# Optimization experiments

Hardware: AMD Instinct MI355X
Metric: run time of the kernel (lower is better)

## Reference

```python
import jax, jax.numpy as jnp
import numpy as np

K = 8        # number of nearest neighbors
STRIDE = 1
PAD = 2      # 'same' padding for kernel_size=5


def setup_inputs() -> dict:
    key = jax.random.key(0)
    k1, k2, k3 = jax.random.split(key, 3)
    x = jax.random.normal(k1, (32, 3, 64, 64), dtype=jnp.float32)
    patches = jax.random.normal(k2, (2048, 3, 5, 5), dtype=jnp.float32)
    values = jax.random.normal(k3, (2048, 128), dtype=jnp.float32)
    return {"x": x, "patches": patches, "values": values}


def reference(x, patches, values):
    # Precompute (as done in NeighborsValuesAssigner.__init__):
    #   kernel = -patches, bias = 0.5 * ||patch||^2
    n = patches.shape[0]
    pf = patches.reshape(n, -1)
    bias = 0.5 * jnp.sum(pf * pf, axis=1)          # (N,)
    kernel = -patches                               # (N, C, kh, kw)

    # distances[b, n, h, w] = -<patch_n, x_patch(b,h,w)> + 0.5*||patch_n||^2
    dist = jax.lax.conv_general_dilated(
        x, kernel,
        window_strides=(STRIDE, STRIDE),
        padding=[(PAD, PAD), (PAD, PAD)],
        dimension_numbers=("NCHW", "OIHW", "NCHW"),
    ) + bias[None, :, None, None]                   # (B, N, H, W)

    # k smallest distances along the dictionary axis
    dist = jnp.transpose(dist, (0, 2, 3, 1))        # (B, H, W, N)
    _, idx = jax.lax.top_k(-dist, K)                # (B, H, W, K)

    # gather neighbor value vectors and mean-reduce over neighbors
    gathered = values[idx]                          # (B, H, W, K, D)
    out = jnp.mean(gathered, axis=3)                # (B, H, W, D)
    return jnp.transpose(out, (0, 3, 1, 2))         # (B, D, H, W)
```

## Files before the change

kernel.cpp:

```cpp
#include <hip/hip_runtime.h>
#include <float.h>

#define B_  32
#define C_  3
#define H_  64
#define W_  64
#define N_  2048
#define D_  128
#define KNN 8
#define PS  75
#define TILES 128
#define CK  12

typedef __attribute__((ext_vector_type(8))) _Float16 kh8;
typedef __attribute__((ext_vector_type(4))) float kvf4;

__global__ __launch_bounds__(256) void bias_kernel(const float* __restrict__ patches,
                                                   float* __restrict__ nbias) {
  int n = blockIdx.x * 256 + threadIdx.x;
  if (n < N_) {
    const float* __restrict__ p = patches + n * PS;
    float s = 0.f;
#pragma unroll
    for (int j = 0; j < PS; j++) s += p[j] * p[j];
    nbias[n] = -0.5f * s;
  }
}

__device__ __forceinline__ void bub12(unsigned (&s)[CK], unsigned c) {
#pragma unroll
  for (int j = 0; j < CK; j++) {
    const unsigned lo = s[j] < c ? s[j] : c;
    const unsigned hi = s[j] < c ? c : s[j];
    s[j] = lo;
    c = hi;
  }
}

__device__ __forceinline__ void ins8(float cd, int ci, float (&rd)[KNN], int (&ri)[KNN]) {
#pragma unroll
  for (int q = 0; q < KNN; q++) {
    const bool sw = (cd < rd[q]) || (cd == rd[q] && ci < ri[q]);
    const float nd = sw ? rd[q] : cd;
    const int   ni = sw ? ri[q] : ci;
    rd[q] = sw ? cd : rd[q];
    ri[q] = sw ? ci : ri[q];
    cd = nd;
    ci = ni;
  }
}

__global__ __launch_bounds__(256)
__attribute__((amdgpu_waves_per_eu(2, 4)))
void knn_kernel(const float* __restrict__ x, const float* __restrict__ patches,
                const float* __restrict__ values, const float* __restrict__ nbias,
                float* __restrict__ out) {
  __shared__ float xt[1633];
  __shared__ float mg_d[4][4][16][KNN];
  __shared__ int   mg_i[4][4][16][KNN];
  __shared__ int   bc_i[4][16][KNN];

  const int tid = threadIdx.x;
  const int bp = blockIdx.x * 256;
  const int b  = bp >> 12;
  const int h0 = (bp >> 6) & 63;

  for (int f = tid; f < 1632; f += 256) {
    const int c   = f / 544;
    const int rem = f - c * 544;
    const int j   = rem / 68;
    const int col = rem - j * 68;
    const int gr = h0 - 2 + j;
    const int gc = col - 2;
    float v = 0.f;
    if ((unsigned)gr < 64u && (unsigned)gc < 64u)
      v = x[((b * 3 + c) * 64 + gr) * 64 + gc];
    xt[f] = v;
  }
  if (tid == 0) xt[1632] = 0.f;
  __syncthreads();

  const int lane = tid & 63;
  const int wid  = tid >> 6;
  const int l15  = lane & 15;
  const int g4   = lane >> 4;

  kh8 bfr[4][3];
  float snorm[4];
#pragma unroll
  for (int g = 0; g < 4; g++) {
    const int pb = wid * 68 + g * 16 + l15;
#pragma unroll
    for (int s = 0; s < 3; s++) {
      union { _Float16 h[8]; kh8 v; } fr;
#pragma unroll
      for (int i = 0; i < 8; i++) {
        const int k  = s * 32 + g4 * 8 + i;
        const int c  = k / 25;
        const int r2 = k - c * 25;
        const int addr = (k < PS) ? (pb + c * 544 + (r2 / 5) * 68 + (r2 % 5)) : 1632;
        fr.h[i] = (_Float16)xt[addr];
      }
      bfr[g][s] = fr.v;
    }
    float sq = 0.f;
#pragma unroll
    for (int c = 0; c < 3; c++)
#pragma unroll
      for (int dh = 0; dh < 5; dh++)
#pragma unroll
        for (int dw = 0; dw < 5; dw++) {
          const _Float16 hv = (_Float16)xt[pb + c * 544 + dh * 68 + dw];
          const float vr = (float)hv;
          sq = fmaf(vr, vr, sq);
        }
    snorm[g] = 0.5f * sq;
  }

  unsigned sk0[CK], sk1[CK], sk2[CK], sk3[CK];
#pragma unroll
  for (int j = 0; j < CK; j++) sk0[j] = sk1[j] = sk2[j] = sk3[j] = 0xFFFFFFFFu;

#pragma unroll 1
  for (int t = 0; t < TILES; t++) {
    const float* __restrict__ pr = patches + (t * 16 + l15) * PS + g4 * 8;
    union { _Float16 h[8]; kh8 v; } af[3];
#pragma unroll
    for (int s = 0; s < 3; s++)
#pragma unroll
      for (int i = 0; i < 8; i++) {
        const int k = s * 32 + g4 * 8 + i;
        const float e = (k < PS) ? pr[s * 32 + i] : 0.f;
        af[s].h[i] = (_Float16)e;
      }

    const int nbb = t * 16 + g4 * 4;
    const float nb0 = nbias[nbb + 0];
    const float nb1 = nbias[nbb + 1];
    const float nb2 = nbias[nbb + 2];
    const float nb3 = nbias[nbb + 3];
    const unsigned tb = (unsigned)nbb;
#pragma unroll
    for (int g = 0; g < 4; g++) {
      kvf4 acc;
      acc[0] = nb0; acc[1] = nb1; acc[2] = nb2; acc[3] = nb3;
      acc = __builtin_amdgcn_mfma_f32_16x16x32_f16(af[0].v, bfr[g][0], acc, 0, 0, 0);
      acc = __builtin_amdgcn_mfma_f32_16x16x32_f16(af[1].v, bfr[g][1], acc, 0, 0, 0);
      acc = __builtin_amdgcn_mfma_f32_16x16x32_f16(af[2].v, bfr[g][2], acc, 0, 0, 0);
#pragma unroll
      for (int r = 0; r < 4; r++) {
        float kv = snorm[g] - acc[r];
        kv = fmaxf(kv, 0.f);
        const unsigned ku = (__float_as_uint(kv) & 0xFFFFF800u) | (tb + (unsigned)r);
        if      (g == 0) bub12(sk0, ku);
        else if (g == 1) bub12(sk1, ku);
        else if (g == 2) bub12(sk2, ku);
        else             bub12(sk3, ku);
      }
    }
  }

#pragma unroll 1
  for (int g = 0; g < 4; g++) {
    float xv[PS];
    const int pb = wid * 68 + g * 16 + l15;
#pragma unroll
    for (int c = 0; c < 3; c++)
#pragma unroll
      for (int dh = 0; dh < 5; dh++)
#pragma unroll
        for (int dw = 0; dw < 5; dw++)
          xv[(c * 5 + dh) * 5 + dw] = xt[pb + c * 544 + dh * 68 + dw];

    float rd[KNN];
    int ri[KNN];
#pragma unroll
    for (int j = 0; j < KNN; j++) { rd[j] = FLT_MAX; ri[j] = 0; }

#pragma unroll 1
    for (int j = 0; j < CK; j++) {
      const unsigned cj = (g == 0) ? sk0[j] : (g == 1) ? sk1[j] : (g == 2) ? sk2[j] : sk3[j];
      const int idx = (int)(cj & 0x7FFu);
      const float* __restrict__ pp = patches + idx * PS;
      float d0 = 0.f, d1 = 0.f, d2 = 0.f, d3 = 0.f;
#pragma unroll
      for (int u = 0; u < 18; u++) {
        d0 = fmaf(pp[4 * u + 0], xv[4 * u + 0], d0);
        d1 = fmaf(pp[4 * u + 1], xv[4 * u + 1], d1);
        d2 = fmaf(pp[4 * u + 2], xv[4 * u + 2], d2);
        d3 = fmaf(pp[4 * u + 3], xv[4 * u + 3], d3);
      }
      d0 = fmaf(pp[72], xv[72], d0);
      d1 = fmaf(pp[73], xv[73], d1);
      d2 = fmaf(pp[74], xv[74], d2);
      const float dot = (d0 + d1) + (d2 + d3);
      const float cd = -(nbias[idx] + dot);
      ins8(cd, idx, rd, ri);
    }

#pragma unroll
    for (int s = 0; s < KNN; s++) {
      mg_d[wid][g4][l15][s] = rd[s];
      mg_i[wid][g4][l15][s] = ri[s];
    }
    __syncthreads();
    if (g4 == 0) {
#pragma unroll
      for (int q = 1; q < 4; q++)
#pragma unroll
        for (int s = 0; s < KNN; s++)
          ins8(mg_d[wid][q][l15][s], mg_i[wid][q][l15][s], rd, ri);
#pragma unroll
      for (int s = 0; s < KNN; s++) bc_i[wid][l15][s] = ri[s];
    }
    __syncthreads();

    int mi[KNN];
#pragma unroll
    for (int s = 0; s < KNN; s++) mi[s] = bc_i[wid][l15][s] & 0x7FF;
    const int obase = ((b * D_ + g4 * 32) * 64 + (h0 + wid)) * 64 + (g * 16 + l15);
#pragma unroll 1
    for (int dd = 0; dd < 32; dd += 4) {
      float s0 = 0.f, s1 = 0.f, s2 = 0.f, s3 = 0.f;
#pragma unroll
      for (int k = 0; k < KNN; k++) {
        const float4 v = *(const float4*)(values + mi[k] * D_ + g4 * 32 + dd);
        s0 += v.x; s1 += v.y; s2 += v.z; s3 += v.w;
      }
      out[obase + (dd + 0) * 4096] = s0 * 0.125f;
      out[obase + (dd + 1) * 4096] = s1 * 0.125f;
      out[obase + (dd + 2) * 4096] = s2 * 0.125f;
      out[obase + (dd + 3) * 4096] = s3 * 0.125f;
    }
  }
}

extern "C" void kernel_launch(void* const* d_in, const int* in_sizes, int n_in,
                              void* d_out, int out_size, void* d_ws, size_t ws_size,
                              hipStream_t stream) {
  const float* x = (const float*)d_in[0];
  const float* patches = (const float*)d_in[1];
  const float* values = (const float*)d_in[2];
  float* out = (float*)d_out;
  float* nbias = (float*)d_ws;

  hipLaunchKernelGGL(bias_kernel, dim3(N_ / 256), dim3(256), 0, stream, patches, nbias);
  hipLaunchKernelGGL(knn_kernel, dim3((B_ * H_ * W_) / 256), dim3(256), 0, stream,
                     x, patches, values, nbias, out);
}
```

Measured before the change: 727.0 us.

## Precompute fp16 MFMA patch fragments and prefetch next tile in the scan loop

Adds a pre-pass kernel that converts patches to fp16 and lays them out in the exact per-lane MFMA A-fragment order in workspace. The main kernel then loads each tile's fragment with three 16-byte loads instead of 24 scalar strided fp32 loads plus conversions, and it software-pipelines the next tile's fragment and bias loads one iteration ahead. This reduces the global load count and conversion ALU work in the hot loop and hides load latency. The cost is an extra small kernel launch, some more live registers, and a duplicated fallback kernel kept for when the workspace is too small.

After: 643.9 us. -11.4%, faster.

```diff
diff --git a/kernel.cpp b/kernel.cpp
--- a/kernel.cpp
+++ b/kernel.cpp
@@ -15,6 +15,8 @@
 typedef __attribute__((ext_vector_type(8))) _Float16 kh8;
 typedef __attribute__((ext_vector_type(4))) float kvf4;
 
+struct FragPOD { unsigned a, b, c, d; };
+
 __global__ __launch_bounds__(256) void bias_kernel(const float* __restrict__ patches,
                                                    float* __restrict__ nbias) {
   int n = blockIdx.x * 256 + threadIdx.x;
@@ -25,6 +27,23 @@
     for (int j = 0; j < PS; j++) s += p[j] * p[j];
     nbias[n] = -0.5f * s;
   }
+}
+
+__global__ __launch_bounds__(192) void pfrag_kernel(const float* __restrict__ patches,
+                                                    FragPOD* __restrict__ pfrag) {
+  const int t = blockIdx.x;
+  const int s = threadIdx.x >> 6;
+  const int l = threadIdx.x & 63;
+  const int m = t * 16 + (l & 15);
+  const int g4 = l >> 4;
+  union { _Float16 h[8]; FragPOD f; } fr;
+#pragma unroll
+  for (int i = 0; i < 8; i++) {
+    const int k = s * 32 + g4 * 8 + i;
+    const float v = (k < PS) ? patches[m * PS + k] : 0.f;
+    fr.h[i] = (_Float16)v;
+  }
+  pfrag[(t * 3 + s) * 64 + l] = fr.f;
 }
 
 __device__ __forceinline__ void bub12(unsigned (&s)[CK], unsigned c) {
@@ -54,7 +73,7 @@
 __attribute__((amdgpu_waves_per_eu(2, 4)))
 void knn_kernel(const float* __restrict__ x, const float* __restrict__ patches,
                 const float* __restrict__ values, const float* __restrict__ nbias,
-                float* __restrict__ out) {
+                const FragPOD* __restrict__ pfrag, float* __restrict__ out) {
   __shared__ float xt[1633];
   __shared__ float mg_d[4][4][16][KNN];
   __shared__ int   mg_i[4][4][16][KNN];
@@ -121,32 +140,37 @@
 #pragma unroll
   for (int j = 0; j < CK; j++) sk0[j] = sk1[j] = sk2[j] = sk3[j] = 0xFFFFFFFFu;
 
+  const unsigned ib = (unsigned)(g4 * 4);
+
+  FragPOD c0 = pfrag[lane];
+  FragPOD c1 = pfrag[64 + lane];
+  FragPOD c2 = pfrag[128 + lane];
+  float nb0 = nbias[g4 * 4 + 0];
+  float nb1 = nbias[g4 * 4 + 1];
+  float nb2 = nbias[g4 * 4 + 2];
+  float nb3 = nbias[g4 * 4 + 3];
+
 #pragma unroll 1
   for (int t = 0; t < TILES; t++) {
-    const float* __restrict__ pr = patches + (t * 16 + l15) * PS + g4 * 8;
-    union { _Float16 h[8]; kh8 v; } af[3];
-#pragma unroll
-    for (int s = 0; s < 3; s++)
-#pragma unroll
-      for (int i = 0; i < 8; i++) {
-        const int k = s * 32 + g4 * 8 + i;
-        const float e = (k < PS) ? pr[s * 32 + i] : 0.f;
-        af[s].h[i] = (_Float16)e;
-      }
-
-    const int nbb = t * 16 + g4 * 4;
-    const float nb0 = nbias[nbb + 0];
-    const float nb1 = nbias[nbb + 1];
-    const float nb2 = nbias[nbb + 2];
-    const float nb3 = nbias[nbb + 3];
-    const unsigned tb = (unsigned)nbb;
+    union { FragPOD f; kh8 v; } a0, a1, a2;
+    a0.f = c0; a1.f = c1; a2.f = c2;
+    const float b0 = nb0, b1 = nb1, b2 = nb2, b3 = nb3;
+
+    const int tn = (t + 1) & (TILES - 1);
+    const FragPOD* __restrict__ pn = pfrag + tn * 192 + lane;
+    c0 = pn[0]; c1 = pn[64]; c2 = pn[128];
+    const int nbn = tn * 16 + g4 * 4;
+    nb0 = nbias[nbn + 0]; nb1 = nbias[nbn + 1];
+    nb2 = nbias[nbn + 2]; nb3 = nbias[nbn + 3];
+
+    const unsigned tb = (unsigned)(t * 16) + ib;
 #pragma unroll
     for (int g = 0; g < 4; g++) {
       kvf4 acc;
-      acc[0] = nb0; acc[1] = nb1; acc[2] = nb2; acc[3] = nb3;
-      acc = __builtin_amdgcn_mfma_f32_16x16x32_f16(af[0].v, bfr[g][0], acc, 0, 0, 0);
-      acc = __builtin_amdgcn_mfma_f32_16x16x32_f16(af[1].v, bfr[g][1], acc, 0, 0, 0);
-      acc = __builtin_amdgcn_mfma_f32_16x16x32_f16(af[2].v, bfr[g][2], acc, 0, 0, 0);
+      acc[0] = b0; acc[1] = b1; acc[2] = b2; acc[3] = b3;
+      acc = __builtin_amdgcn_mfma_f32_16x16x32_f16(a0.v, bfr[g][0], acc, 0, 0, 0);
+      acc = __builtin_amdgcn_mfma_f32_16x16x32_f16(a1.v, bfr[g][1], acc, 0, 0, 0);
+      acc = __builtin_amdgcn_mfma_f32_16x16x32_f16(a2.v, bfr[g][2], acc, 0, 0, 0);
 #pragma unroll
       for (int r = 0; r < 4; r++) {
         float kv = snorm[g] - acc[r];
@@ -235,6 +259,191 @@
   }
 }
 
+__global__ __launch_bounds__(256)
+__attribute__((amdgpu_waves_per_eu(2, 4)))
+void knn_fallback(const float* __restrict__ x, const float* __restrict__ patches,
+                  const float* __restrict__ values, const float* __restrict__ nbias,
+                  float* __restrict__ out) {
+  __shared__ float xt[1633];
+  __shared__ float mg_d[4][4][16][KNN];
+  __shared__ int   mg_i[4][4][16][KNN];
+  __shared__ int   bc_i[4][16][KNN];
+
+  const int tid = threadIdx.x;
+  const int bp = blockIdx.x * 256;
+  const int b  = bp >> 12;
+  const int h0 = (bp >> 6) & 63;
+
+  for (int f = tid; f < 1632; f += 256) {
+    const int c   = f / 544;
+    const int rem = f - c * 544;
+    const int j   = rem / 68;
+    const int col = rem - j * 68;
+    const int gr = h0 - 2 + j;
+    const int gc = col - 2;
+    float v = 0.f;
+    if ((unsigned)gr < 64u && (unsigned)gc < 64u)
+      v = x[((b * 3 + c) * 64 + gr) * 64 + gc];
+    xt[f] = v;
+  }
+  if (tid == 0) xt[1632] = 0.f;
+  __syncthreads();
+
+  const int lane = tid & 63;
+  const int wid  = tid >> 6;
+  const int l15  = lane & 15;
+  const int g4   = lane >> 4;
+
+  kh8 bfr[4][3];
+  float snorm[4];
+#pragma unroll
+  for (int g = 0; g < 4; g++) {
+    const int pb = wid * 68 + g * 16 + l15;
+#pragma unroll
+    for (int s = 0; s < 3; s++) {
+      union { _Float16 h[8]; kh8 v; } fr;
+#pragma unroll
+      for (int i = 0; i < 8; i++) {
+        const int k  = s * 32 + g4 * 8 + i;
+        const int c  = k / 25;
+        const int r2 = k - c * 25;
+        const int addr = (k < PS) ? (pb + c * 544 + (r2 / 5) * 68 + (r2 % 5)) : 1632;
+        fr.h[i] = (_Float16)xt[addr];
+      }
+      bfr[g][s] = fr.v;
+    }
+    float sq = 0.f;
+#pragma unroll
+    for (int c = 0; c < 3; c++)
+#pragma unroll
+      for (int dh = 0; dh < 5; dh++)
+#pragma unroll
+        for (int dw = 0; dw < 5; dw++) {
+          const _Float16 hv = (_Float16)xt[pb + c * 544 + dh * 68 + dw];
+          const float vr = (float)hv;
+          sq = fmaf(vr, vr, sq);
+        }
+    snorm[g] = 0.5f * sq;
+  }
+
+  unsigned sk0[CK], sk1[CK], sk2[CK], sk3[CK];
+#pragma unroll
+  for (int j = 0; j < CK; j++) sk0[j] = sk1[j] = sk2[j] = sk3[j] = 0xFFFFFFFFu;
+
+#pragma unroll 1
+  for (int t = 0; t < TILES; t++) {
+    const float* __restrict__ pr = patches + (t * 16 + l15) * PS + g4 * 8;
+    union { _Float16 h[8]; kh8 v; } af[3];
+#pragma unroll
+    for (int s = 0; s < 3; s++)
+#pragma unroll
+      for (int i = 0; i < 8; i++) {
+        const int k = s * 32 + g4 * 8 + i;
+        const float e = (k < PS) ? pr[s * 32 + i] : 0.f;
+        af[s].h[i] = (_Float16)e;
+      }
+
+    const int nbb = t * 16 + g4 * 4;
+    const float nb0 = nbias[nbb + 0];
+    const float nb1 = nbias[nbb + 1];
+    const float nb2 = nbias[nbb + 2];
+    const float nb3 = nbias[nbb + 3];
+    const unsigned tb = (unsigned)nbb;
+#pragma unroll
+    for (int g = 0; g < 4; g++) {
+      kvf4 acc;
+      acc[0] = nb0; acc[1] = nb1; acc[2] = nb2; acc[3] = nb3;
+      acc = __builtin_amdgcn_mfma_f32_16x16x32_f16(af[0].v, bfr[g][0], acc, 0, 0, 0);
+      acc = __builtin_amdgcn_mfma_f32_16x16x32_f16(af[1].v, bfr[g][1], acc, 0, 0, 0);
+      acc = __builtin_amdgcn_mfma_f32_16x16x32_f16(af[2].v, bfr[g][2], acc, 0, 0, 0);
+#pragma unroll
+      for (int r = 0; r < 4; r++) {
+        float kv = snorm[g] - acc[r];
+        kv = fmaxf(kv, 0.f);
+        const unsigned ku = (__float_as_uint(kv) & 0xFFFFF800u) | (tb + (unsigned)r);
+        if      (g == 0) bub12(sk0, ku);
+        else if (g == 1) bub12(sk1, ku);
+        else if (g == 2) bub12(sk2, ku);
+        else             bub12(sk3, ku);
+      }
+    }
+  }
+
+#pragma unroll 1
+  for (int g = 0; g < 4; g++) {
+    float xv[PS];
+    const int pb = wid * 68 + g * 16 + l15;
+#pragma unroll
+    for (int c = 0; c < 3; c++)
+#pragma unroll
+      for (int dh = 0; dh < 5; dh++)
+#pragma unroll
+        for (int dw = 0; dw < 5; dw++)
+          xv[(c * 5 + dh) * 5 + dw] = xt[pb + c * 544 + dh * 68 + dw];
+
+    float rd[KNN];
+    int ri[KNN];
+#pragma unroll
+    for (int j = 0; j < KNN; j++) { rd[j] = FLT_MAX; ri[j] = 0; }
+
+#pragma unroll 1
+    for (int j = 0; j < CK; j++) {
+      const unsigned cj = (g == 0) ? sk0[j] : (g == 1) ? sk1[j] : (g == 2) ? sk2[j] : sk3[j];
+      const int idx = (int)(cj & 0x7FFu);
+      const float* __restrict__ pp = patches + idx * PS;
+      float d0 = 0.f, d1 = 0.f, d2 = 0.f, d3 = 0.f;
+#pragma unroll
+      for (int u = 0; u < 18; u++) {
+        d0 = fmaf(pp[4 * u + 0], xv[4 * u + 0], d0);
+        d1 = fmaf(pp[4 * u + 1], xv[4 * u + 1], d1);
+        d2 = fmaf(pp[4 * u + 2], xv[4 * u + 2], d2);
+        d3 = fmaf(pp[4 * u + 3], xv[4 * u + 3], d3);
+      }
+      d0 = fmaf(pp[72], xv[72], d0);
+      d1 = fmaf(pp[73], xv[73], d1);
+      d2 = fmaf(pp[74], xv[74], d2);
+      const float dot = (d0 + d1) + (d2 + d3);
+      const float cd = -(nbias[idx] + dot);
+      ins8(cd, idx, rd, ri);
+    }
+
+#pragma unroll
+    for (int s = 0; s < KNN; s++) {
+      mg_d[wid][g4][l15][s] = rd[s];
+      mg_i[wid][g4][l15][s] = ri[s];
+    }
+    __syncthreads();
+    if (g4 == 0) {
+#pragma unroll
+      for (int q = 1; q < 4; q++)
+#pragma unroll
+        for (int s = 0; s < KNN; s++)
+          ins8(mg_d[wid][q][l15][s], mg_i[wid][q][l15][s], rd, ri);
+#pragma unroll
+      for (int s = 0; s < KNN; s++) bc_i[wid][l15][s] = ri[s];
+    }
+    __syncthreads();
+
+    int mi[KNN];
+#pragma unroll
+    for (int s = 0; s < KNN; s++) mi[s] = bc_i[wid][l15][s] & 0x7FF;
+    const int obase = ((b * D_ + g4 * 32) * 64 + (h0 + wid)) * 64 + (g * 16 + l15);
+#pragma unroll 1
+    for (int dd = 0; dd < 32; dd += 4) {
+      float s0 = 0.f, s1 = 0.f, s2 = 0.f, s3 = 0.f;
+#pragma unroll
+      for (int k = 0; k < KNN; k++) {
+        const float4 v = *(const float4*)(values + mi[k] * D_ + g4 * 32 + dd);
+        s0 += v.x; s1 += v.y; s2 += v.z; s3 += v.w;
+      }
+      out[obase + (dd + 0) * 4096] = s0 * 0.125f;
+      out[obase + (dd + 1) * 4096] = s1 * 0.125f;
+      out[obase + (dd + 2) * 4096] = s2 * 0.125f;
+      out[obase + (dd + 3) * 4096] = s3 * 0.125f;
+    }
+  }
+}
+
 extern "C" void kernel_launch(void* const* d_in, const int* in_sizes, int n_in,
                               void* d_out, int out_size, void* d_ws, size_t ws_size,
                               hipStream_t stream) {
@@ -242,9 +451,21 @@
   const float* patches = (const float*)d_in[1];
   const float* values = (const float*)d_in[2];
   float* out = (float*)d_out;
-  float* nbias = (float*)d_ws;
-
-  hipLaunchKernelGGL(bias_kernel, dim3(N_ / 256), dim3(256), 0, stream, patches, nbias);
-  hipLaunchKernelGGL(knn_kernel, dim3((B_ * H_ * W_) / 256), dim3(256), 0, stream,
-                     x, patches, values, nbias, out);
-}
+
+  const size_t PFRAG_B = (size_t)TILES * 3 * 64 * 16;
+  const size_t BIAS_B  = (size_t)N_ * 4;
+
+  if (ws_size >= PFRAG_B + BIAS_B) {
+    FragPOD* pfrag = (FragPOD*)d_ws;
+    float* nbias   = (float*)((char*)d_ws + PFRAG_B);
+    hipLaunchKernelGGL(bias_kernel, dim3(N_ / 256), dim3(256), 0, stream, patches, nbias);
+    hipLaunchKernelGGL(pfrag_kernel, dim3(TILES), dim3(192), 0, stream, patches, pfrag);
+    hipLaunchKernelGGL(knn_kernel, dim3((B_ * H_ * W_) / 256), dim3(256), 0, stream,
+                       x, patches, values, nbias, pfrag, out);
+  } else {
+    float* nbias = (float*)d_ws;
+    hipLaunchKernelGGL(bias_kernel, dim3(N_ / 256), dim3(256), 0, stream, patches, nbias);
+    hipLaunchKernelGGL(knn_fallback, dim3((B_ * H_ * W_) / 256), dim3(256), 0, stream,
+                       x, patches, values, nbias, out);
+  }
+}
```
